# Kernel tuning notes

Measured on AMD Instinct MI355X. Metric: run time of the kernel, lower is better.

The kernel has to match this reference:

```python
import jax, jax.numpy as jnp
import numpy as np

V, D, H, L, E = 50000, 128, 128, 4, 160000


def setup_inputs() -> dict:
    key = jax.random.key(0)
    ks = jax.random.split(key, 8)
    inp = {
        "node_embeddings": jax.random.normal(ks[0], (V, D), dtype=jnp.float32),
        "adj0": jax.random.randint(ks[1], (E, 2), 0, V, dtype=jnp.int32),
        "adj1": jax.random.randint(ks[2], (E, 2), 0, V, dtype=jnp.int32),
        "adj2": jax.random.randint(ks[3], (E, 2), 0, V, dtype=jnp.int32),
        "adj3": jax.random.randint(ks[4], (E, 2), 0, V, dtype=jnp.int32),
        # One MLP per (edge_type, endpoint): Linear(2D->H) -> relu -> Linear(H->H), no biases
        "W1": jax.random.normal(ks[5], (L, 2, 2 * D, H), dtype=jnp.float32) * 0.05,
        "W2": jax.random.normal(ks[6], (L, 2, H, H), dtype=jnp.float32) * 0.05,
    }
    return inp


def reference(node_embeddings, adj0, adj1, adj2, adj3, W1, W2):
    num_nodes = node_embeddings.shape[0]
    msgs = []
    tgts = []
    for l, adj in enumerate((adj0, adj1, adj2, adj3)):
        # gather both endpoint states and concat -> [E, 2D]
        src = node_embeddings[adj[:, 0]]
        dst = node_embeddings[adj[:, 1]]
        raw = jnp.concatenate([src, dst], axis=-1)
        # one MLP per endpoint; messages sent to that endpoint's node
        for ep in range(2):
            h = jax.nn.relu(raw @ W1[l, ep])          # [E, H]
            msgs.append(h @ W2[l, ep])                 # [E, H]
            tgts.append(adj[:, ep])
    messages = jnp.concatenate(msgs, axis=0)          # [L*2*E, H]
    targets = jnp.concatenate(tgts, axis=0)           # [L*2*E]
    agg = jax.ops.segment_sum(messages, targets, num_segments=num_nodes)  # [V, H]
    return jax.nn.relu(agg)
```

## Files before the change

kernel.cpp:

```cpp
#include <hip/hip_runtime.h>

#define V_NODES 50000
#define NEDGE   160000
#define NSEG    (8 * V_NODES)

typedef __bf16 bf16;
typedef __attribute__((ext_vector_type(8))) __bf16 bf16x8;
typedef __attribute__((ext_vector_type(4))) __bf16 bf16x4;
typedef __attribute__((ext_vector_type(2))) __bf16 bf16x2;
typedef __attribute__((ext_vector_type(4))) float  f32x4;

__device__ __forceinline__ int clampV(int n) {
  unsigned u = (unsigned)n;
  return (int)(u < (unsigned)V_NODES ? u : (unsigned)(V_NODES - 1));
}

__device__ __forceinline__ float bflo(unsigned u) {
  return __builtin_bit_cast(float, u << 16);
}
__device__ __forceinline__ float bfhi(unsigned u) {
  return __builtin_bit_cast(float, u & 0xffff0000u);
}


__global__ __launch_bounds__(256) void prep_emb_k(const float* __restrict__ in,
                                                  bf16* __restrict__ out) {
  int i = blockIdx.x * 256 + threadIdx.x;
  float4 v = ((const float4*)in)[i];
  bf16x4 o = {(bf16)v.x, (bf16)v.y, (bf16)v.z, (bf16)v.w};
  *(bf16x4*)(out + (size_t)i * 4) = o;
}

__global__ __launch_bounds__(256) void prep_w1_k(const float* __restrict__ in,
                                                 bf16* __restrict__ out) {
  int idx = blockIdx.x * 256 + threadIdx.x;
  int n = idx & 127, k = (idx >> 7) & 255, g = idx >> 15;
  out[(((g << 7) + n) << 8) + k] = (bf16)in[idx];
}

__global__ __launch_bounds__(256) void prep_w2_k(const float* __restrict__ in,
                                                 bf16* __restrict__ out) {
  int idx = blockIdx.x * 256 + threadIdx.x;
  int n = idx & 127, k = (idx >> 7) & 127, g = idx >> 14;
  out[(((g << 7) + n) << 7) + k] = (bf16)in[idx];
}

__global__ __launch_bounds__(256) void relu_k(float* __restrict__ out) {
  int i = blockIdx.x * 256 + threadIdx.x;
  float4 v = ((float4*)out)[i];
  v.x = fmaxf(v.x, 0.f); v.y = fmaxf(v.y, 0.f);
  v.z = fmaxf(v.z, 0.f); v.w = fmaxf(v.w, 0.f);
  ((float4*)out)[i] = v;
}


__global__ __launch_bounds__(256) void hist_k(
    const int* __restrict__ a0, const int* __restrict__ a1,
    const int* __restrict__ a2, const int* __restrict__ a3,
    int* __restrict__ counts) {
  int e = blockIdx.x * 256 + threadIdx.x;
  int g = blockIdx.y;
  int l = g >> 1, ep = g & 1;
  const int* adj = (l == 0) ? a0 : (l == 1) ? a1 : (l == 2) ? a2 : a3;
  int tgt = clampV(adj[2 * e + ep]);
  atomicAdd(&counts[g * V_NODES + tgt], 1);
}

__global__ __launch_bounds__(256) void scan_a_k(const int* __restrict__ counts,
                                                int* __restrict__ offs,
                                                int* __restrict__ bsums) {
  __shared__ int sh[256];
  int t = threadIdx.x, base = blockIdx.x * 512;
  int e0 = base + 2 * t, e1 = e0 + 1;
  int a = (e0 < NSEG) ? counts[e0] : 0;
  int b = (e1 < NSEG) ? counts[e1] : 0;
  int s = a + b;
  sh[t] = s;
  __syncthreads();
  #pragma unroll
  for (int d = 1; d < 256; d <<= 1) {
    int v = (t >= d) ? sh[t - d] : 0;
    __syncthreads();
    sh[t] += v;
    __syncthreads();
  }
  int excl = sh[t] - s;
  if (e0 < NSEG) offs[e0] = excl;
  if (e1 < NSEG) offs[e1] = excl + a;
  if (t == 255) bsums[blockIdx.x] = sh[255];
}

#define NBLK_SCAN 782

__global__ __launch_bounds__(256) void scan_b_k(int* __restrict__ bsums,
                                                int* __restrict__ offs) {
  __shared__ int sh[NBLK_SCAN];
  int t = threadIdx.x;
  for (int i = t; i < NBLK_SCAN; i += 256) sh[i] = bsums[i];
  __syncthreads();
  if (t == 0) {
    int run = 0;
    for (int i = 0; i < NBLK_SCAN; ++i) { int v = sh[i]; sh[i] = run; run += v; }
    offs[NSEG] = run;
  }
  __syncthreads();
  for (int i = t; i < NBLK_SCAN; i += 256) bsums[i] = sh[i];
}

__global__ __launch_bounds__(256) void scan_c_k(int* __restrict__ offs,
                                                const int* __restrict__ bsums) {
  int i = blockIdx.x * 256 + threadIdx.x;
  if (i < NSEG) offs[i] += bsums[i >> 9];
}

__global__ __launch_bounds__(256) void scatter_ids2_k(
    const int* __restrict__ a0, const int* __restrict__ a1,
    const int* __restrict__ a2, const int* __restrict__ a3,
    const int* __restrict__ offs, int* __restrict__ cursor,
    int2* __restrict__ ids2) {
  int e = blockIdx.x * 256 + threadIdx.x;
  int g = blockIdx.y;
  int l = g >> 1, ep = g & 1;
  const int* adj = (l == 0) ? a0 : (l == 1) ? a1 : (l == 2) ? a2 : a3;
  int2 pr = ((const int2*)adj)[e];
  int src = clampV(pr.x), dst = clampV(pr.y);
  int tgt = ep ? dst : src;
  int seg = g * V_NODES + tgt;
  int pos = offs[seg] + atomicAdd(&cursor[seg], 1);
  ids2[pos] = make_int2(src, dst);
}


__global__ __launch_bounds__(256) void xgemm2_k(const bf16* __restrict__ embB,
                                                const bf16* __restrict__ w1t,
                                                bf16* __restrict__ Xab,
                                                int gbase) {
  const int tid = threadIdx.x, w = tid >> 6, lane = tid & 63;
  const int l15 = lane & 15, q = lane >> 4;
  const int h2 = w >> 1, dh = w & 1;
  const int slot = blockIdx.y, g = gbase + slot;

  bf16x8 wA[4][4];
  const bf16* __restrict__ w1g = w1t + (size_t)g * 32768;
  #pragma unroll
  for (int mb = 0; mb < 4; ++mb)
    #pragma unroll
    for (int kb = 0; kb < 4; ++kb)
      wA[mb][kb] = *(const bf16x8*)(w1g + (size_t)(dh * 64 + mb * 16 + l15) * 256 +
                                    h2 * 128 + kb * 32 + q * 8);

  bf16* __restrict__ Xh = Xab + (size_t)slot * 12800000 + (size_t)h2 * 6400000;

  #pragma unroll
  for (int t = 0; t < 5; ++t) {
    const int node = blockIdx.x * 80 + t * 16 + l15;
    bf16x8 b[4];
    #pragma unroll
    for (int kb = 0; kb < 4; ++kb)
      b[kb] = *(const bf16x8*)(embB + (size_t)node * 128 + kb * 32 + q * 8);

    f32x4 acc[4] = {};
    #pragma unroll
    for (int kb = 0; kb < 4; ++kb)
      #pragma unroll
      for (int mb = 0; mb < 4; ++mb)
        acc[mb] = __builtin_amdgcn_mfma_f32_16x16x32_bf16(wA[mb][kb], b[kb], acc[mb], 0, 0, 0);

    bf16* basep = Xh + (size_t)node * 128 + dh * 64 + q * 4;
    #pragma unroll
    for (int mb = 0; mb < 4; ++mb) {
      bf16x4 o = {(bf16)acc[mb][0], (bf16)acc[mb][1],
                  (bf16)acc[mb][2], (bf16)acc[mb][3]};
      *(bf16x4*)(basep + mb * 16) = o;
    }
  }
}


__global__ __launch_bounds__(256) void aggf4_k(
    const bf16* __restrict__ Xab,
    const int* __restrict__ offs, const int2* __restrict__ ids2,
    bf16* __restrict__ HaggB, int gbase) {
  const int wv = threadIdx.x >> 6, lane = threadIdx.x & 63;
  const int h = lane >> 5, m = lane & 31;
  const int node = blockIdx.x * 8 + wv * 2 + h;
  const int slot = blockIdx.y, g = gbase + slot;
  const int ep = g & 1;
  const bf16* __restrict__ Xa = Xab + (size_t)slot * 12800000;
  const bf16* __restrict__ Xb = Xa + 6400000;
  const bf16* __restrict__ own = ep ? Xb : Xa;
  const bf16* __restrict__ oth = ep ? Xa : Xb;
  const int seg = g * V_NODES + node;
  const int beg = offs[seg], end = offs[seg + 1];

  uint2 uo = *(const uint2*)(own + (size_t)node * 128 + m * 4);
  const float o0 = bflo(uo.x), o1 = bfhi(uo.x);
  const float o2 = bflo(uo.y), o3 = bfhi(uo.y);

  float s0 = 0.f, s1 = 0.f, s2 = 0.f, s3 = 0.f;
  int i = beg;
  for (; i + 2 <= end; i += 2) {
    int2 p0 = ids2[i];
    int2 p1 = ids2[i + 1];
    int n0 = ep ? p0.x : p0.y;
    int n1 = ep ? p1.x : p1.y;
    uint2 u0 = *(const uint2*)(oth + (size_t)n0 * 128 + m * 4);
    uint2 u1 = *(const uint2*)(oth + (size_t)n1 * 128 + m * 4);
    s0 += fmaxf(o0 + bflo(u0.x), 0.f) + fmaxf(o0 + bflo(u1.x), 0.f);
    s1 += fmaxf(o1 + bfhi(u0.x), 0.f) + fmaxf(o1 + bfhi(u1.x), 0.f);
    s2 += fmaxf(o2 + bflo(u0.y), 0.f) + fmaxf(o2 + bflo(u1.y), 0.f);
    s3 += fmaxf(o3 + bfhi(u0.y), 0.f) + fmaxf(o3 + bfhi(u1.y), 0.f);
  }
  if (i < end) {
    int2 p = ids2[i];
    int n = ep ? p.x : p.y;
    uint2 u = *(const uint2*)(oth + (size_t)n * 128 + m * 4);
    s0 += fmaxf(o0 + bflo(u.x), 0.f);
    s1 += fmaxf(o1 + bfhi(u.x), 0.f);
    s2 += fmaxf(o2 + bflo(u.y), 0.f);
    s3 += fmaxf(o3 + bfhi(u.y), 0.f);
  }
  bf16x4 st = {(bf16)s0, (bf16)s1, (bf16)s2, (bf16)s3};
  *(bf16x4*)(HaggB + ((size_t)g * V_NODES + node) * 128 + m * 4) = st;
}


__global__ __launch_bounds__(256) void gemm2p_k(const bf16* __restrict__ HaggB,
                                                const bf16* __restrict__ w2t,
                                                float* __restrict__ out) {
  __shared__ __attribute__((aligned(16))) bf16 a_lds[32 * 128];

  const int tid = threadIdx.x, wv = tid >> 6, lane = tid & 63;
  const int l15 = lane & 15, q = lane >> 4;
  const int v0 = blockIdx.x * 32;

  const int srow = tid >> 3, sc0 = (tid & 7) * 2;
  bf16* sp0 = &a_lds[srow * 128 + ((sc0 ^ (srow & 7)) << 3)];
  bf16* sp1 = &a_lds[srow * 128 + (((sc0 + 1) ^ (srow & 7)) << 3)];

  const uint4* Hg = (const uint4*)(HaggB + (size_t)v0 * 128);
  uint4 s0 = Hg[tid * 2], s1 = Hg[tid * 2 + 1];

  f32x4 acc[2][2] = {};
  for (int g = 0; g < 8; ++g) {
    __syncthreads();
    *(uint4*)sp0 = s0;
    *(uint4*)sp1 = s1;
    if (g < 7) {
      const uint4* Hn = (const uint4*)(HaggB + (size_t)(g + 1) * 6400000 +
                                       (size_t)v0 * 128);
      s0 = Hn[tid * 2];
      s1 = Hn[tid * 2 + 1];
    }
    __syncthreads();

    const bf16* __restrict__ Wb = w2t + (size_t)g * 16384;
    #pragma unroll
    for (int kb = 0; kb < 4; ++kb) {
      bf16x8 a[2];
      #pragma unroll
      for (int mt = 0; mt < 2; ++mt) {
        int r = mt * 16 + l15;
        a[mt] = *(const bf16x8*)(&a_lds[r * 128 + (((kb * 4 + q) ^ (r & 7)) << 3)]);
      }
      #pragma unroll
      for (int t = 0; t < 2; ++t) {
        int n = (wv * 2 + t) * 16 + l15;
        bf16x8 b = *(const bf16x8*)(Wb + (size_t)n * 128 + kb * 32 + q * 8);
        #pragma unroll
        for (int mt = 0; mt < 2; ++mt)
          acc[mt][t] = __builtin_amdgcn_mfma_f32_16x16x32_bf16(a[mt], b, acc[mt][t], 0, 0, 0);
      }
    }
  }

  #pragma unroll
  for (int mt = 0; mt < 2; ++mt)
    #pragma unroll
    for (int r = 0; r < 4; ++r) {
      int row = v0 + mt * 16 + q * 4 + r;
      if (row < V_NODES) {
        #pragma unroll
        for (int t = 0; t < 2; ++t) {
          int col = (wv * 2 + t) * 16 + l15;
          out[(size_t)row * 128 + col] = fmaxf(acc[mt][t][r], 0.f);
        }
      }
    }
}


__global__ __launch_bounds__(256) void edge_k(
    const bf16* __restrict__ embB,
    const int* __restrict__ a0, const int* __restrict__ a1,
    const int* __restrict__ a2, const int* __restrict__ a3,
    const bf16* __restrict__ w1t, const bf16* __restrict__ w2t,
    float* __restrict__ out) {

  __shared__ __attribute__((aligned(16))) bf16 w1_lds[128 * 256];
  __shared__ __attribute__((aligned(16))) bf16 h_lds[64 * 128];

  const int tid = threadIdx.x;
  const int g  = blockIdx.x >> 6;
  const int bs = blockIdx.x & 63;
  const int l = g >> 1, ep = g & 1;
  const int* __restrict__ adj = (l == 0) ? a0 : (l == 1) ? a1 : (l == 2) ? a2 : a3;

  {
    const uint4* w1g = (const uint4*)(w1t + (size_t)g * 128 * 256);
    #pragma unroll
    for (int i = 0; i < 16; ++i) {
      int j = i * 256 + tid;
      int n = j >> 5, c = j & 31;
      *(uint4*)(&w1_lds[n * 256 + ((c ^ (n & 7)) << 3)]) = w1g[j];
    }
  }
  __syncthreads();

  const int w    = tid >> 6;
  const int lane = tid & 63;
  const int wr = w >> 1, wc = w & 1;
  const int l15 = lane & 15, q = lane >> 4;
  const bf16* __restrict__ w2g = w2t + (size_t)g * 128 * 128;

  for (int t = bs; t < 2500; t += 64) {
    const int ebase = t * 64;
    int2 pr0 = ((const int2*)adj)[ebase + 32 * wr + l15];
    int2 pr1 = ((const int2*)adj)[ebase + 32 * wr + 16 + l15];
    pr0.x = clampV(pr0.x); pr0.y = clampV(pr0.y);
    pr1.x = clampV(pr1.x); pr1.y = clampV(pr1.y);

    f32x4 acc[2][4] = {};
    #pragma unroll
    for (int kb = 0; kb < 8; ++kb) {
      const int k = kb * 32 + q * 8;
      const int klo = k & 127;
      const int n0 = (kb < 4) ? pr0.x : pr0.y;
      const int n1 = (kb < 4) ? pr1.x : pr1.y;
      bf16x8 a[2], b[4];
      a[0] = *(const bf16x8*)(embB + (size_t)n0 * 128 + klo);
      a[1] = *(const bf16x8*)(embB + (size_t)n1 * 128 + klo);
      const int csw = ((kb << 2) + q);
      #pragma unroll
      for (int nt = 0; nt < 4; ++nt) {
        int n = 64 * wc + 16 * nt + l15;
        b[nt] = *(const bf16x8*)(&w1_lds[n * 256 + ((csw ^ (l15 & 7)) << 3)]);
      }
      #pragma unroll
      for (int mt = 0; mt < 2; ++mt)
        #pragma unroll
        for (int nt = 0; nt < 4; ++nt)
          acc[mt][nt] = __builtin_amdgcn_mfma_f32_16x16x32_bf16(a[mt], b[nt], acc[mt][nt], 0, 0, 0);
    }

    __syncthreads();
    #pragma unroll
    for (int mt = 0; mt < 2; ++mt)
      #pragma unroll
      for (int nt = 0; nt < 4; ++nt)
        #pragma unroll
        for (int r = 0; r < 4; ++r) {
          float v = acc[mt][nt][r];
          v = v > 0.f ? v : 0.f;
          int row = 32 * wr + 16 * mt + 4 * q + r;
          int col = 64 * wc + 16 * nt + l15;
          int c = col >> 3;
          h_lds[row * 128 + (((c ^ (row & 7)) << 3) | (col & 7))] = (bf16)v;
        }
    __syncthreads();

    f32x4 acc2[2][4] = {};
    #pragma unroll
    for (int kb = 0; kb < 4; ++kb) {
      const int k = kb * 32 + q * 8;
      const int csw = (kb << 2) + q;
      bf16x8 a[2], b[4];
      #pragma unroll
      for (int mt = 0; mt < 2; ++mt) {
        int row = 32 * wr + 16 * mt + l15;
        a[mt] = *(const bf16x8*)(&h_lds[row * 128 + ((csw ^ (row & 7)) << 3)]);
      }
      #pragma unroll
      for (int nt = 0; nt < 4; ++nt) {
        int n = 64 * wc + 16 * nt + l15;
        b[nt] = *(const bf16x8*)(w2g + n * 128 + k);
      }
      #pragma unroll
      for (int mt = 0; mt < 2; ++mt)
        #pragma unroll
        for (int nt = 0; nt < 4; ++nt)
          acc2[mt][nt] = __builtin_amdgcn_mfma_f32_16x16x32_bf16(a[mt], b[nt], acc2[mt][nt], 0, 0, 0);
    }

    #pragma unroll
    for (int mt = 0; mt < 2; ++mt)
      #pragma unroll
      for (int r = 0; r < 4; ++r) {
        int row = 32 * wr + 16 * mt + 4 * q + r;
        int2 pr = ((const int2*)adj)[ebase + row];
        int node = clampV(ep ? pr.y : pr.x);
        float* basep = out + (size_t)node * 128 + 64 * wc + l15;
        #pragma unroll
        for (int nt = 0; nt < 4; ++nt)
          unsafeAtomicAdd(basep + 16 * nt, acc2[mt][nt][r]);
      }
  }
}


extern "C" void kernel_launch(void* const* d_in, const int* in_sizes, int n_in,
                              void* d_out, int out_size, void* d_ws, size_t ws_size,
                              hipStream_t stream) {
  const float* emb = (const float*)d_in[0];
  const int* a0 = (const int*)d_in[1];
  const int* a1 = (const int*)d_in[2];
  const int* a2 = (const int*)d_in[3];
  const int* a3 = (const int*)d_in[4];
  const float* W1 = (const float*)d_in[5];
  const float* W2 = (const float*)d_in[6];
  float* out = (float*)d_out;

  char* ws = (char*)d_ws;
  bf16* embB   = (bf16*)(ws);
  bf16* w1t    = (bf16*)(ws + 12800000);
  bf16* w2t    = (bf16*)(ws + 13324288);
  int*  offs   = (int*) (ws + 13586432);
  int2* ids2   = (int2*)(ws + 15186448);
  int*  bsums  = (int*) (ws + 25426448);
  int*  counts = (int*) (ws + 25429584);
  bf16* HaggB  = (bf16*)(ws + 27029584);
  bf16* Xab    = (bf16*)(ws + 129429584);
  const size_t fixedsz = 129429584;

  prep_emb_k<<<6250, 256, 0, stream>>>(emb, embB);
  prep_w1_k<<<1024, 256, 0, stream>>>(W1, w1t);
  prep_w2_k<<<512, 256, 0, stream>>>(W2, w2t);

  int GG = 0;
  if      (ws_size >= fixedsz + 8ull * 25600000) GG = 8;
  else if (ws_size >= fixedsz + 4ull * 25600000) GG = 4;
  else if (ws_size >= fixedsz + 2ull * 25600000) GG = 2;
  else if (ws_size >= fixedsz + 1ull * 25600000) GG = 1;

  if (GG) {
    hipMemsetAsync(counts, 0, 1600000, stream);
    hist_k<<<dim3(625, 8), 256, 0, stream>>>(a0, a1, a2, a3, counts);
    scan_a_k<<<NBLK_SCAN, 256, 0, stream>>>(counts, offs, bsums);
    scan_b_k<<<1, 256, 0, stream>>>(bsums, offs);
    scan_c_k<<<1563, 256, 0, stream>>>(offs, bsums);
    hipMemsetAsync(counts, 0, 1600000, stream);
    scatter_ids2_k<<<dim3(625, 8), 256, 0, stream>>>(a0, a1, a2, a3, offs, counts, ids2);

    for (int gb = 0; gb < 8; gb += GG) {
      xgemm2_k<<<dim3(625, GG), 256, 0, stream>>>(embB, w1t, Xab, gb);
      aggf4_k<<<dim3(6250, GG), 256, 0, stream>>>(Xab, offs, ids2, HaggB, gb);
    }
    gemm2p_k<<<1563, 256, 0, stream>>>(HaggB, w2t, out);
  } else {
    hipMemsetAsync(d_out, 0, 25600000, stream);
    edge_k<<<512, 256, 0, stream>>>(embB, a0, a1, a2, a3, w1t, w2t, out);
    relu_k<<<6250, 256, 0, stream>>>(out);
  }
}
```

Baseline: 504.0 us.

## Fuse prep, histogram and scatter kernels; store single neighbor id per edge

Merges the embedding/weight conversion kernels and the histogram into one launch, and runs the id scatter inside the first X-GEMM launch so the two overlap. The scatter now bumps the scanned offsets array (shifted by one) in place as its cursor, which removes the second memset and the separate cursor buffer. Each edge stores only the other endpoint's id (int instead of int2), halving index traffic in the aggregation. Fewer launches and less memory traffic are traded for an atomic-cursor scheme whose correctness depends on the shifted-offset trick.

```diff
diff --git a/kernel.cpp b/kernel.cpp
--- a/kernel.cpp
+++ b/kernel.cpp
@@ -7,7 +7,6 @@
 typedef __bf16 bf16;
 typedef __attribute__((ext_vector_type(8))) __bf16 bf16x8;
 typedef __attribute__((ext_vector_type(4))) __bf16 bf16x4;
-typedef __attribute__((ext_vector_type(2))) __bf16 bf16x2;
 typedef __attribute__((ext_vector_type(4))) float  f32x4;
 
 __device__ __forceinline__ int clampV(int n) {
@@ -54,20 +53,41 @@
 }
 
 
-__global__ __launch_bounds__(256) void hist_k(
+__global__ __launch_bounds__(256) void fused_prep_k(
+    const float* __restrict__ emb, const float* __restrict__ W1,
+    const float* __restrict__ W2,
     const int* __restrict__ a0, const int* __restrict__ a1,
     const int* __restrict__ a2, const int* __restrict__ a3,
+    bf16* __restrict__ embB, bf16* __restrict__ w1t, bf16* __restrict__ w2t,
     int* __restrict__ counts) {
-  int e = blockIdx.x * 256 + threadIdx.x;
-  int g = blockIdx.y;
-  int l = g >> 1, ep = g & 1;
-  const int* adj = (l == 0) ? a0 : (l == 1) ? a1 : (l == 2) ? a2 : a3;
-  int tgt = clampV(adj[2 * e + ep]);
-  atomicAdd(&counts[g * V_NODES + tgt], 1);
-}
+  const int bx = blockIdx.x, tid = threadIdx.x;
+  if (bx < 6250) {
+    int i = bx * 256 + tid;
+    float4 v = ((const float4*)emb)[i];
+    bf16x4 o = {(bf16)v.x, (bf16)v.y, (bf16)v.z, (bf16)v.w};
+    *(bf16x4*)(embB + (size_t)i * 4) = o;
+  } else if (bx < 7274) {
+    int idx = (bx - 6250) * 256 + tid;
+    int n = idx & 127, k = (idx >> 7) & 255, g = idx >> 15;
+    w1t[(((g << 7) + n) << 8) + k] = (bf16)W1[idx];
+  } else if (bx < 7786) {
+    int idx = (bx - 7274) * 256 + tid;
+    int n = idx & 127, k = (idx >> 7) & 127, g = idx >> 14;
+    w2t[(((g << 7) + n) << 7) + k] = (bf16)W2[idx];
+  } else {
+    int j = bx - 7786;
+    int g = j / 625;
+    int e = (j - g * 625) * 256 + tid;
+    int l = g >> 1, ep = g & 1;
+    const int* adj = (l == 0) ? a0 : (l == 1) ? a1 : (l == 2) ? a2 : a3;
+    int tgt = clampV(adj[2 * e + ep]);
+    atomicAdd(&counts[g * V_NODES + tgt], 1);
+  }
+}
+
 
 __global__ __launch_bounds__(256) void scan_a_k(const int* __restrict__ counts,
-                                                int* __restrict__ offs,
+                                                int* __restrict__ offs1,
                                                 int* __restrict__ bsums) {
   __shared__ int sh[256];
   int t = threadIdx.x, base = blockIdx.x * 512;
@@ -85,15 +105,15 @@
     __syncthreads();
   }
   int excl = sh[t] - s;
-  if (e0 < NSEG) offs[e0] = excl;
-  if (e1 < NSEG) offs[e1] = excl + a;
+  if (e0 < NSEG) offs1[e0] = excl;
+  if (e1 < NSEG) offs1[e1] = excl + a;
   if (t == 255) bsums[blockIdx.x] = sh[255];
 }
 
 #define NBLK_SCAN 782
 
 __global__ __launch_bounds__(256) void scan_b_k(int* __restrict__ bsums,
-                                                int* __restrict__ offs) {
+                                                int* __restrict__ offsX) {
   __shared__ int sh[NBLK_SCAN];
   int t = threadIdx.x;
   for (int i = t; i < NBLK_SCAN; i += 256) sh[i] = bsums[i];
@@ -101,85 +121,88 @@
   if (t == 0) {
     int run = 0;
     for (int i = 0; i < NBLK_SCAN; ++i) { int v = sh[i]; sh[i] = run; run += v; }
-    offs[NSEG] = run;
+    offsX[0] = 0;
   }
   __syncthreads();
   for (int i = t; i < NBLK_SCAN; i += 256) bsums[i] = sh[i];
 }
 
-__global__ __launch_bounds__(256) void scan_c_k(int* __restrict__ offs,
+__global__ __launch_bounds__(256) void scan_c_k(int* __restrict__ offs1,
                                                 const int* __restrict__ bsums) {
   int i = blockIdx.x * 256 + threadIdx.x;
-  if (i < NSEG) offs[i] += bsums[i >> 9];
-}
-
-__global__ __launch_bounds__(256) void scatter_ids2_k(
+  if (i < NSEG) offs1[i] += bsums[i >> 9];
+}
+
+
+__global__ __launch_bounds__(256) void fused_xg_sc_k(
+    const bf16* __restrict__ embB, const bf16* __restrict__ w1t,
+    bf16* __restrict__ Xab,
     const int* __restrict__ a0, const int* __restrict__ a1,
     const int* __restrict__ a2, const int* __restrict__ a3,
-    const int* __restrict__ offs, int* __restrict__ cursor,
-    int2* __restrict__ ids2) {
-  int e = blockIdx.x * 256 + threadIdx.x;
-  int g = blockIdx.y;
-  int l = g >> 1, ep = g & 1;
-  const int* adj = (l == 0) ? a0 : (l == 1) ? a1 : (l == 2) ? a2 : a3;
-  int2 pr = ((const int2*)adj)[e];
-  int src = clampV(pr.x), dst = clampV(pr.y);
-  int tgt = ep ? dst : src;
-  int seg = g * V_NODES + tgt;
-  int pos = offs[seg] + atomicAdd(&cursor[seg], 1);
-  ids2[pos] = make_int2(src, dst);
-}
-
-
-__global__ __launch_bounds__(256) void xgemm2_k(const bf16* __restrict__ embB,
-                                                const bf16* __restrict__ w1t,
-                                                bf16* __restrict__ Xab,
-                                                int gbase) {
-  const int tid = threadIdx.x, w = tid >> 6, lane = tid & 63;
-  const int l15 = lane & 15, q = lane >> 4;
-  const int h2 = w >> 1, dh = w & 1;
-  const int slot = blockIdx.y, g = gbase + slot;
-
-  bf16x8 wA[4][4];
-  const bf16* __restrict__ w1g = w1t + (size_t)g * 32768;
-  #pragma unroll
-  for (int mb = 0; mb < 4; ++mb)
-    #pragma unroll
-    for (int kb = 0; kb < 4; ++kb)
-      wA[mb][kb] = *(const bf16x8*)(w1g + (size_t)(dh * 64 + mb * 16 + l15) * 256 +
-                                    h2 * 128 + kb * 32 + q * 8);
-
-  bf16* __restrict__ Xh = Xab + (size_t)slot * 12800000 + (size_t)h2 * 6400000;
-
-  #pragma unroll
-  for (int t = 0; t < 5; ++t) {
-    const int node = blockIdx.x * 80 + t * 16 + l15;
-    bf16x8 b[4];
-    #pragma unroll
-    for (int kb = 0; kb < 4; ++kb)
-      b[kb] = *(const bf16x8*)(embB + (size_t)node * 128 + kb * 32 + q * 8);
-
-    f32x4 acc[4] = {};
-    #pragma unroll
-    for (int kb = 0; kb < 4; ++kb)
-      #pragma unroll
-      for (int mb = 0; mb < 4; ++mb)
-        acc[mb] = __builtin_amdgcn_mfma_f32_16x16x32_bf16(wA[mb][kb], b[kb], acc[mb], 0, 0, 0);
-
-    bf16* basep = Xh + (size_t)node * 128 + dh * 64 + q * 4;
-    #pragma unroll
-    for (int mb = 0; mb < 4; ++mb) {
-      bf16x4 o = {(bf16)acc[mb][0], (bf16)acc[mb][1],
-                  (bf16)acc[mb][2], (bf16)acc[mb][3]};
-      *(bf16x4*)(basep + mb * 16) = o;
-    }
+    int* __restrict__ offs1, int* __restrict__ ids,
+    int gbase, int nxg) {
+  const int tid = threadIdx.x;
+  if ((int)blockIdx.x < nxg) {
+    const int slot = blockIdx.x / 625;
+    const int bxx  = blockIdx.x - slot * 625;
+    const int w = tid >> 6, lane = tid & 63;
+    const int l15 = lane & 15, q = lane >> 4;
+    const int h2 = w >> 1, dh = w & 1;
+    const int g = gbase + slot;
+
+    bf16x8 wA[4][4];
+    const bf16* __restrict__ w1g = w1t + (size_t)g * 32768;
+    #pragma unroll
+    for (int mb = 0; mb < 4; ++mb)
+      #pragma unroll
+      for (int kb = 0; kb < 4; ++kb)
+        wA[mb][kb] = *(const bf16x8*)(w1g + (size_t)(dh * 64 + mb * 16 + l15) * 256 +
+                                      h2 * 128 + kb * 32 + q * 8);
+
+    bf16* __restrict__ Xh = Xab + (size_t)slot * 12800000 + (size_t)h2 * 6400000;
+
+    #pragma unroll
+    for (int t = 0; t < 5; ++t) {
+      const int node = bxx * 80 + t * 16 + l15;
+      bf16x8 b[4];
+      #pragma unroll
+      for (int kb = 0; kb < 4; ++kb)
+        b[kb] = *(const bf16x8*)(embB + (size_t)node * 128 + kb * 32 + q * 8);
+
+      f32x4 acc[4] = {};
+      #pragma unroll
+      for (int kb = 0; kb < 4; ++kb)
+        #pragma unroll
+        for (int mb = 0; mb < 4; ++mb)
+          acc[mb] = __builtin_amdgcn_mfma_f32_16x16x32_bf16(wA[mb][kb], b[kb], acc[mb], 0, 0, 0);
+
+      bf16* basep = Xh + (size_t)node * 128 + dh * 64 + q * 4;
+      #pragma unroll
+      for (int mb = 0; mb < 4; ++mb) {
+        bf16x4 o = {(bf16)acc[mb][0], (bf16)acc[mb][1],
+                    (bf16)acc[mb][2], (bf16)acc[mb][3]};
+        *(bf16x4*)(basep + mb * 16) = o;
+      }
+    }
+  } else {
+    int j = blockIdx.x - nxg;
+    int g = j / 625;
+    int e = (j - g * 625) * 256 + tid;
+    int l = g >> 1, ep = g & 1;
+    const int* adj = (l == 0) ? a0 : (l == 1) ? a1 : (l == 2) ? a2 : a3;
+    int2 pr = ((const int2*)adj)[e];
+    int src = clampV(pr.x), dst = clampV(pr.y);
+    int tgt = ep ? dst : src;
+    int oth = ep ? src : dst;
+    int pos = atomicAdd(&offs1[g * V_NODES + tgt], 1);
+    ids[pos] = oth;
   }
 }
 
 
 __global__ __launch_bounds__(256) void aggf4_k(
     const bf16* __restrict__ Xab,
-    const int* __restrict__ offs, const int2* __restrict__ ids2,
+    const int* __restrict__ offsX, const int* __restrict__ ids,
     bf16* __restrict__ HaggB, int gbase) {
   const int wv = threadIdx.x >> 6, lane = threadIdx.x & 63;
   const int h = lane >> 5, m = lane & 31;
@@ -191,7 +214,7 @@
   const bf16* __restrict__ own = ep ? Xb : Xa;
   const bf16* __restrict__ oth = ep ? Xa : Xb;
   const int seg = g * V_NODES + node;
-  const int beg = offs[seg], end = offs[seg + 1];
+  const int beg = offsX[seg], end = offsX[seg + 1];
 
   uint2 uo = *(const uint2*)(own + (size_t)node * 128 + m * 4);
   const float o0 = bflo(uo.x), o1 = bfhi(uo.x);
@@ -200,10 +223,8 @@
   float s0 = 0.f, s1 = 0.f, s2 = 0.f, s3 = 0.f;
   int i = beg;
   for (; i + 2 <= end; i += 2) {
-    int2 p0 = ids2[i];
-    int2 p1 = ids2[i + 1];
-    int n0 = ep ? p0.x : p0.y;
-    int n1 = ep ? p1.x : p1.y;
+    int n0 = ids[i];
+    int n1 = ids[i + 1];
     uint2 u0 = *(const uint2*)(oth + (size_t)n0 * 128 + m * 4);
     uint2 u1 = *(const uint2*)(oth + (size_t)n1 * 128 + m * 4);
     s0 += fmaxf(o0 + bflo(u0.x), 0.f) + fmaxf(o0 + bflo(u1.x), 0.f);
@@ -212,8 +233,7 @@
     s3 += fmaxf(o3 + bfhi(u0.y), 0.f) + fmaxf(o3 + bfhi(u1.y), 0.f);
   }
   if (i < end) {
-    int2 p = ids2[i];
-    int n = ep ? p.x : p.y;
+    int n = ids[i];
     uint2 u = *(const uint2*)(oth + (size_t)n * 128 + m * 4);
     s0 += fmaxf(o0 + bflo(u.x), 0.f);
     s1 += fmaxf(o1 + bfhi(u.x), 0.f);
@@ -424,17 +444,14 @@
   bf16* embB   = (bf16*)(ws);
   bf16* w1t    = (bf16*)(ws + 12800000);
   bf16* w2t    = (bf16*)(ws + 13324288);
-  int*  offs   = (int*) (ws + 13586432);
-  int2* ids2   = (int2*)(ws + 15186448);
-  int*  bsums  = (int*) (ws + 25426448);
-  int*  counts = (int*) (ws + 25429584);
-  bf16* HaggB  = (bf16*)(ws + 27029584);
-  bf16* Xab    = (bf16*)(ws + 129429584);
-  const size_t fixedsz = 129429584;
-
-  prep_emb_k<<<6250, 256, 0, stream>>>(emb, embB);
-  prep_w1_k<<<1024, 256, 0, stream>>>(W1, w1t);
-  prep_w2_k<<<512, 256, 0, stream>>>(W2, w2t);
+  int*  offsX  = (int*) (ws + 13586432);
+  int*  ids    = (int*) (ws + 15186448);
+  int*  bsums  = (int*) (ws + 20306448);
+  int*  counts = (int*) (ws + 20309584);
+  bf16* HaggB  = (bf16*)(ws + 21909584);
+  bf16* Xab    = (bf16*)(ws + 124309584);
+  const size_t fixedsz = 124309584;
+  int* offs1 = offsX + 1;
 
   int GG = 0;
   if      (ws_size >= fixedsz + 8ull * 25600000) GG = 8;
@@ -444,19 +461,26 @@
 
   if (GG) {
     hipMemsetAsync(counts, 0, 1600000, stream);
-    hist_k<<<dim3(625, 8), 256, 0, stream>>>(a0, a1, a2, a3, counts);
-    scan_a_k<<<NBLK_SCAN, 256, 0, stream>>>(counts, offs, bsums);
-    scan_b_k<<<1, 256, 0, stream>>>(bsums, offs);
-    scan_c_k<<<1563, 256, 0, stream>>>(offs, bsums);
-    hipMemsetAsync(counts, 0, 1600000, stream);
-    scatter_ids2_k<<<dim3(625, 8), 256, 0, stream>>>(a0, a1, a2, a3, offs, counts, ids2);
-
-    for (int gb = 0; gb < 8; gb += GG) {
-      xgemm2_k<<<dim3(625, GG), 256, 0, stream>>>(embB, w1t, Xab, gb);
-      aggf4_k<<<dim3(6250, GG), 256, 0, stream>>>(Xab, offs, ids2, HaggB, gb);
+    fused_prep_k<<<12786, 256, 0, stream>>>(emb, W1, W2, a0, a1, a2, a3,
+                                            embB, w1t, w2t, counts);
+    scan_a_k<<<NBLK_SCAN, 256, 0, stream>>>(counts, offs1, bsums);
+    scan_b_k<<<1, 256, 0, stream>>>(bsums, offsX);
+    scan_c_k<<<1563, 256, 0, stream>>>(offs1, bsums);
+
+    fused_xg_sc_k<<<625 * GG + 5000, 256, 0, stream>>>(
+        embB, w1t, Xab, a0, a1, a2, a3, offs1, ids, 0, 625 * GG);
+    aggf4_k<<<dim3(6250, GG), 256, 0, stream>>>(Xab, offsX, ids, HaggB, 0);
+
+    for (int gb = GG; gb < 8; gb += GG) {
+      fused_xg_sc_k<<<625 * GG, 256, 0, stream>>>(
+          embB, w1t, Xab, a0, a1, a2, a3, offs1, ids, gb, 625 * GG);
+      aggf4_k<<<dim3(6250, GG), 256, 0, stream>>>(Xab, offsX, ids, HaggB, gb);
     }
     gemm2p_k<<<1563, 256, 0, stream>>>(HaggB, w2t, out);
   } else {
+    prep_emb_k<<<6250, 256, 0, stream>>>(emb, embB);
+    prep_w1_k<<<1024, 256, 0, stream>>>(W1, w1t);
+    prep_w2_k<<<512, 256, 0, stream>>>(W2, w2t);
     hipMemsetAsync(d_out, 0, 25600000, stream);
     edge_k<<<512, 256, 0, stream>>>(embB, a0, a1, a2, a3, w1t, w2t, out);
     relu_k<<<6250, 256, 0, stream>>>(out);
```

Result: no change. 507.2 us (+0.6%).
